# Kernel tuning notes

Hardware: AMD Instinct MI355X
Metric: run time of the kernel (lower is better)

The kernel has to match this reference:

```python
import jax, jax.numpy as jnp
import numpy as np
from jax.scipy.special import logsumexp

F = 200000   # numFactors
V = 100000   # numVars
S = 5        # state_dimensions (binary vars -> factor tables are (2,)*S)
E = 1000000  # number of factor-to-variable edges


def setup_inputs() -> dict:
    key = jax.random.key(0)
    ks = jax.random.split(key, 8)
    shape_f = (F,) + (2,) * S
    return {
        "factor_beliefs": jax.random.normal(ks[0], shape_f, jnp.float32),
        "var_beliefs": jax.random.normal(ks[1], (V, 2), jnp.float32),
        "factor_potentials": jax.random.normal(ks[2], shape_f, jnp.float32),
        "prv_varToFactor_messages": jax.random.normal(ks[3], (E, 2), jnp.float32),
        "prv_factorToVar_messages": jax.random.normal(ks[4], (E, 2), jnp.float32),
        "f2v_factor_idx": jax.random.randint(ks[5], (E,), 0, F),
        "f2v_var_idx": jax.random.randint(ks[6], (E,), 0, V),
        "edge_var_idx": jax.random.randint(ks[7], (E,), 0, S),
    }


def _bp_iteration(factor_beliefs, var_beliefs, factor_potentials,
                  prv_v2f, prv_f2v, f_idx, v_idx, ev_idx):
    nF = factor_beliefs.shape[0]
    nV = var_beliefs.shape[0]
    nS = factor_beliefs.ndim - 1  # state_dimensions

    # ---- message_factorToVar ----
    mapped_f = factor_beliefs[f_idx]  # [E, 2,...,2] gather along edges
    # logsumexp over all factor axes except each candidate axis d -> [E, S, 2]
    lse_per_axis = jnp.stack(
        [logsumexp(mapped_f, axis=tuple(a for a in range(1, nS + 1) if a != d + 1))
         for d in range(nS)], axis=1)
    # pick per-edge the axis this edge's variable occupies -> [E, 2]
    marg = jnp.take_along_axis(lse_per_axis, ev_idx[:, None, None], axis=1)[:, 0, :]
    f2v_msgs = marg - jnp.where(jnp.isneginf(prv_v2f), 0.0, prv_v2f)

    # ---- var beliefs: scatter-add over edges, then per-var normalization ----
    var_b = jax.ops.segment_sum(f2v_msgs, v_idx, num_segments=nV)
    var_b = var_b - logsumexp(var_b, axis=1, keepdims=True)

    # ---- message_varToFactor ----
    mapped_v = var_b[v_idx]  # [E, 2]
    v2f_msgs = mapped_v - jnp.where(jnp.isneginf(prv_f2v), 0.0, prv_f2v)

    # ---- expand each [2] message along its per-edge factor axis -> [E, 2^S] ----
    # expanded[e, i0..i_{S-1}] = msg[e, i_{ev_idx[e]}]
    idx_grid = jnp.indices((2,) * nS).reshape(nS, -1)  # [S, 2^S] coord along each axis
    sel = idx_grid[ev_idx]                              # [E, 2^S]
    expanded = jnp.take_along_axis(v2f_msgs, sel, axis=1)  # [E, 2^S]

    # ---- factor beliefs: scatter-add, add potentials, normalize per factor ----
    fb = jax.ops.segment_sum(expanded, f_idx, num_segments=nF)
    fb = fb.reshape((nF,) + (2,) * nS) + factor_potentials
    fb_flat = fb.reshape(nF, -1)
    fb = (fb_flat - logsumexp(fb_flat, axis=1, keepdims=True)).reshape(fb.shape)

    return var_b, fb, f2v_msgs, v2f_msgs


def reference(factor_beliefs, var_beliefs, factor_potentials,
              prv_varToFactor_messages, prv_factorToVar_messages,
              f2v_factor_idx, f2v_var_idx, edge_var_idx):
    # Returns (new var_beliefs, new factor_beliefs,
    #          prv_factorToVar_messages', prv_varToFactor_messages')
    return _bp_iteration(factor_beliefs, var_beliefs, factor_potentials,
                         prv_varToFactor_messages, prv_factorToVar_messages,
                         f2v_factor_idx, f2v_var_idx, edge_var_idx)
```

## Files before the change

kernel.cpp:

```cpp
#include <hip/hip_runtime.h>
#include <math.h>

__global__ void __launch_bounds__(256) k0_flse(
    const float* __restrict__ fbel,
    float* __restrict__ flse,
    int F)
{
    int f = blockIdx.x * 256 + threadIdx.x;
    if (f >= F) return;

    const float4* tab = reinterpret_cast<const float4*>(fbel + (size_t)f * 32);
    float v[32];
#pragma unroll
    for (int q = 0; q < 8; ++q) {
        float4 t = tab[q];
        v[q*4+0] = t.x; v[q*4+1] = t.y; v[q*4+2] = t.z; v[q*4+3] = t.w;
    }

    float m = v[0];
#pragma unroll
    for (int j = 1; j < 32; ++j) m = fmaxf(m, v[j]);

    float s[10];
#pragma unroll
    for (int i = 0; i < 10; ++i) s[i] = 0.f;
#pragma unroll
    for (int j = 0; j < 32; ++j) {
        float ex = __expf(v[j] - m);
#pragma unroll
        for (int d = 0; d < 5; ++d) s[d*2 + ((j >> (4 - d)) & 1)] += ex;
    }

    float* o = flse + (size_t)f * 10;
#pragma unroll
    for (int i = 0; i < 10; ++i) o[i] = m + __logf(s[i]);
}

__global__ void __launch_bounds__(256) k1_f2v(
    const float* __restrict__ flse,
    const float* __restrict__ pv2f,
    const int*   __restrict__ fidx,
    const int*   __restrict__ vidx,
    const int*   __restrict__ evidx,
    float* __restrict__ f2v_out,
    float* __restrict__ vacc,
    int E)
{
    int e = blockIdx.x * 256 + threadIdx.x;
    if (e >= E) return;
    int f = fidx[e], d = evidx[e];

    float2 lse = *reinterpret_cast<const float2*>(flse + (size_t)f * 10 + d * 2);
    float2 p   = *reinterpret_cast<const float2*>(pv2f + 2 * (size_t)e);
    float p0 = (p.x == -INFINITY) ? 0.f : p.x;
    float p1 = (p.y == -INFINITY) ? 0.f : p.y;
    float r0 = lse.x - p0, r1 = lse.y - p1;

    *reinterpret_cast<float2*>(f2v_out + 2 * (size_t)e) = make_float2(r0, r1);

    int vi = vidx[e];
    atomicAdd(&vacc[2*vi],   r0);
    atomicAdd(&vacc[2*vi+1], r1);
}

__global__ void __launch_bounds__(256) k2_varnorm(float* __restrict__ vb, int V)
{
    int v = blockIdx.x * 256 + threadIdx.x;
    if (v >= V) return;
    float a0 = vb[2*v], a1 = vb[2*v+1];
    float m = fmaxf(a0, a1);
    float l = m + __logf(__expf(a0 - m) + __expf(a1 - m));
    vb[2*v]   = a0 - l;
    vb[2*v+1] = a1 - l;
}

__global__ void __launch_bounds__(256) k3_v2f(
    const float* __restrict__ vb,
    const float* __restrict__ pf2v,
    const int*   __restrict__ fidx,
    const int*   __restrict__ vidx,
    const int*   __restrict__ evidx,
    float* __restrict__ v2f_out,
    float* __restrict__ facc,
    int E)
{
    int e = blockIdx.x * 256 + threadIdx.x;
    if (e >= E) return;
    int vi = vidx[e];
    float2 b = *reinterpret_cast<const float2*>(vb + 2 * (size_t)vi);
    float2 p = *reinterpret_cast<const float2*>(pf2v + 2 * (size_t)e);
    float p0 = (p.x == -INFINITY) ? 0.f : p.x;
    float p1 = (p.y == -INFINITY) ? 0.f : p.y;
    float r0 = b.x - p0, r1 = b.y - p1;

    *reinterpret_cast<float2*>(v2f_out + 2 * (size_t)e) = make_float2(r0, r1);

    int f = fidx[e], d = evidx[e];
    atomicAdd(&facc[(size_t)f*10 + d*2    ], r0);
    atomicAdd(&facc[(size_t)f*10 + d*2 + 1], r1);
}

__global__ void __launch_bounds__(256) k4_fb(
    const float* __restrict__ facc,
    const float* __restrict__ pot,
    float* __restrict__ fb_out,
    int F)
{
    int f = blockIdx.x * 256 + threadIdx.x;
    if (f >= F) return;

    float a[10];
#pragma unroll
    for (int i = 0; i < 10; ++i) a[i] = facc[(size_t)f*10 + i];

    float t[32];
    const float4* pp = reinterpret_cast<const float4*>(pot + (size_t)f * 32);
#pragma unroll
    for (int q = 0; q < 8; ++q) {
        float4 x = pp[q];
        t[q*4+0] = x.x; t[q*4+1] = x.y; t[q*4+2] = x.z; t[q*4+3] = x.w;
    }

    float m = -INFINITY;
#pragma unroll
    for (int j = 0; j < 32; ++j) {
        float s = t[j];
#pragma unroll
        for (int d = 0; d < 5; ++d) s += a[d*2 + ((j >> (4 - d)) & 1)];
        t[j] = s;
        m = fmaxf(m, s);
    }
    float sum = 0.f;
#pragma unroll
    for (int j = 0; j < 32; ++j) sum += __expf(t[j] - m);
    float l = m + __logf(sum);

    float4* out = reinterpret_cast<float4*>(fb_out + (size_t)f * 32);
#pragma unroll
    for (int q = 0; q < 8; ++q) {
        float4 x;
        x.x = t[q*4+0] - l; x.y = t[q*4+1] - l;
        x.z = t[q*4+2] - l; x.w = t[q*4+3] - l;
        out[q] = x;
    }
}

extern "C" void kernel_launch(void* const* d_in, const int* in_sizes, int n_in,
                              void* d_out, int out_size, void* d_ws, size_t ws_size,
                              hipStream_t stream)
{
    const float* fbel  = (const float*)d_in[0];
    const float* pot   = (const float*)d_in[2];
    const float* pv2f  = (const float*)d_in[3];
    const float* pf2v  = (const float*)d_in[4];
    const int*   fidx  = (const int*)d_in[5];
    const int*   vidx  = (const int*)d_in[6];
    const int*   evidx = (const int*)d_in[7];

    const int E  = in_sizes[5];
    const int F_ = in_sizes[0] / 32;
    const int V_ = in_sizes[1] / 2;

    float* out     = (float*)d_out;
    float* var_out = out;
    float* fb_out  = out + (size_t)V_ * 2;
    float* f2v_out = fb_out + (size_t)F_ * 32;
    float* v2f_out = f2v_out + (size_t)E * 2;

    float* flse = v2f_out;
    float* facc = (float*)d_ws;

    hipMemsetAsync(var_out, 0, (size_t)V_ * 2 * sizeof(float), stream);
    hipMemsetAsync(facc,    0, (size_t)F_ * 10 * sizeof(float), stream);

    k0_flse   <<<dim3((F_ + 255) / 256), dim3(256), 0, stream>>>(fbel, flse, F_);
    k1_f2v    <<<dim3((E  + 255) / 256), dim3(256), 0, stream>>>(
        flse, pv2f, fidx, vidx, evidx, f2v_out, var_out, E);
    k2_varnorm<<<dim3((V_ + 255) / 256), dim3(256), 0, stream>>>(var_out, V_);
    k3_v2f    <<<dim3((E  + 255) / 256), dim3(256), 0, stream>>>(
        var_out, pf2v, fidx, vidx, evidx, v2f_out, facc, E);
    k4_fb     <<<dim3((F_ + 255) / 256), dim3(256), 0, stream>>>(
        facc, pot, fb_out, F_);
}
```

Measured before the change: 347.8 us.

## Replicate scatter accumulators per XCC and use workgroup-scope atomics

Gives each XCC (read from the hardware register) its own copy of the variable and factor accumulators. The scatter atomics then run at workgroup scope, so they can resolve in the XCC-local L2 instead of being made coherent across the whole device. The normalization kernels sum the 8 replicas before normalizing. In exchange the zero-fill of the workspace grows eightfold and the reduce kernels read eight times more data. Correctness depends on workgroup-scope global atomics from different workgroups on the same XCC staying coherent in L2. The new path is taken only when the workspace is large enough.

```diff
diff --git a/kernel.cpp b/kernel.cpp
--- a/kernel.cpp
+++ b/kernel.cpp
@@ -1,5 +1,18 @@
 #include <hip/hip_runtime.h>
 #include <math.h>
+
+__device__ __forceinline__ int xcc_id() {
+    int x;
+    asm volatile("s_getreg_b32 %0, hwreg(HW_REG_XCC_ID)" : "=s"(x));
+    return x & 7;
+}
+
+__device__ __forceinline__ void atom_add(float* p, float v, int use_local) {
+    if (use_local)
+        __hip_atomic_fetch_add(p, v, __ATOMIC_RELAXED, __HIP_MEMORY_SCOPE_WORKGROUP);
+    else
+        __hip_atomic_fetch_add(p, v, __ATOMIC_RELAXED, __HIP_MEMORY_SCOPE_AGENT);
+}
 
 __global__ void __launch_bounds__(256) k0_flse(
     const float* __restrict__ fbel,
@@ -43,13 +56,16 @@
     const int*   __restrict__ vidx,
     const int*   __restrict__ evidx,
     float* __restrict__ f2v_out,
-    float* __restrict__ vacc,
+    float* __restrict__ vacc_rep,
+    long  vstride,
+    int   use_local,
     int E)
 {
     int e = blockIdx.x * 256 + threadIdx.x;
     if (e >= E) return;
+    float* vacc = vacc_rep + (use_local ? (size_t)xcc_id() * vstride : 0);
+
     int f = fidx[e], d = evidx[e];
-
     float2 lse = *reinterpret_cast<const float2*>(flse + (size_t)f * 10 + d * 2);
     float2 p   = *reinterpret_cast<const float2*>(pv2f + 2 * (size_t)e);
     float p0 = (p.x == -INFINITY) ? 0.f : p.x;
@@ -59,19 +75,26 @@
     *reinterpret_cast<float2*>(f2v_out + 2 * (size_t)e) = make_float2(r0, r1);
 
     int vi = vidx[e];
-    atomicAdd(&vacc[2*vi],   r0);
-    atomicAdd(&vacc[2*vi+1], r1);
-}
-
-__global__ void __launch_bounds__(256) k2_varnorm(float* __restrict__ vb, int V)
+    atom_add(&vacc[2 * (size_t)vi],     r0, use_local);
+    atom_add(&vacc[2 * (size_t)vi + 1], r1, use_local);
+}
+
+__global__ void __launch_bounds__(256) k2_varnorm(
+    const float* __restrict__ vacc_rep,
+    float* __restrict__ var_out,
+    int V, int R, long vstride)
 {
     int v = blockIdx.x * 256 + threadIdx.x;
     if (v >= V) return;
-    float a0 = vb[2*v], a1 = vb[2*v+1];
+    float a0 = 0.f, a1 = 0.f;
+    for (int r = 0; r < R; ++r) {
+        float2 t = *reinterpret_cast<const float2*>(vacc_rep + (size_t)r * vstride + 2 * (size_t)v);
+        a0 += t.x; a1 += t.y;
+    }
     float m = fmaxf(a0, a1);
     float l = m + __logf(__expf(a0 - m) + __expf(a1 - m));
-    vb[2*v]   = a0 - l;
-    vb[2*v+1] = a1 - l;
+    var_out[2*v]   = a0 - l;
+    var_out[2*v+1] = a1 - l;
 }
 
 __global__ void __launch_bounds__(256) k3_v2f(
@@ -81,11 +104,15 @@
     const int*   __restrict__ vidx,
     const int*   __restrict__ evidx,
     float* __restrict__ v2f_out,
-    float* __restrict__ facc,
+    float* __restrict__ facc_rep,
+    long  fstride,
+    int   use_local,
     int E)
 {
     int e = blockIdx.x * 256 + threadIdx.x;
     if (e >= E) return;
+    float* facc = facc_rep + (use_local ? (size_t)xcc_id() * fstride : 0);
+
     int vi = vidx[e];
     float2 b = *reinterpret_cast<const float2*>(vb + 2 * (size_t)vi);
     float2 p = *reinterpret_cast<const float2*>(pf2v + 2 * (size_t)e);
@@ -96,22 +123,27 @@
     *reinterpret_cast<float2*>(v2f_out + 2 * (size_t)e) = make_float2(r0, r1);
 
     int f = fidx[e], d = evidx[e];
-    atomicAdd(&facc[(size_t)f*10 + d*2    ], r0);
-    atomicAdd(&facc[(size_t)f*10 + d*2 + 1], r1);
+    atom_add(&facc[(size_t)f * 10 + d * 2],     r0, use_local);
+    atom_add(&facc[(size_t)f * 10 + d * 2 + 1], r1, use_local);
 }
 
 __global__ void __launch_bounds__(256) k4_fb(
-    const float* __restrict__ facc,
+    const float* __restrict__ facc_rep,
     const float* __restrict__ pot,
     float* __restrict__ fb_out,
-    int F)
+    int F, int R, long fstride)
 {
     int f = blockIdx.x * 256 + threadIdx.x;
     if (f >= F) return;
 
     float a[10];
 #pragma unroll
-    for (int i = 0; i < 10; ++i) a[i] = facc[(size_t)f*10 + i];
+    for (int i = 0; i < 10; ++i) a[i] = 0.f;
+    for (int r = 0; r < R; ++r) {
+        const float* src = facc_rep + (size_t)r * fstride + (size_t)f * 10;
+#pragma unroll
+        for (int i = 0; i < 10; ++i) a[i] += src[i];
+    }
 
     float t[32];
     const float4* pp = reinterpret_cast<const float4*>(pot + (size_t)f * 32);
@@ -168,17 +200,25 @@
     float* v2f_out = f2v_out + (size_t)E * 2;
 
     float* flse = v2f_out;
-    float* facc = (float*)d_ws;
-
-    hipMemsetAsync(var_out, 0, (size_t)V_ * 2 * sizeof(float), stream);
-    hipMemsetAsync(facc,    0, (size_t)F_ * 10 * sizeof(float), stream);
+
+    const long V2  = (long)V_ * 2;
+    const long F10 = (long)F_ * 10;
+
+    int R = (ws_size >= (size_t)8 * (size_t)(V2 + F10) * sizeof(float)) ? 8 : 1;
+    int use_local = (R == 8) ? 1 : 0;
+    float* vacc_rep = (float*)d_ws;
+    float* facc_rep = vacc_rep + (size_t)R * V2;
+
+    (void)hipMemsetAsync(d_ws, 0, (size_t)R * (size_t)(V2 + F10) * sizeof(float),
+                         stream);
 
     k0_flse   <<<dim3((F_ + 255) / 256), dim3(256), 0, stream>>>(fbel, flse, F_);
     k1_f2v    <<<dim3((E  + 255) / 256), dim3(256), 0, stream>>>(
-        flse, pv2f, fidx, vidx, evidx, f2v_out, var_out, E);
-    k2_varnorm<<<dim3((V_ + 255) / 256), dim3(256), 0, stream>>>(var_out, V_);
+        flse, pv2f, fidx, vidx, evidx, f2v_out, vacc_rep, V2, use_local, E);
+    k2_varnorm<<<dim3((V_ + 255) / 256), dim3(256), 0, stream>>>(
+        vacc_rep, var_out, V_, R, V2);
     k3_v2f    <<<dim3((E  + 255) / 256), dim3(256), 0, stream>>>(
-        var_out, pf2v, fidx, vidx, evidx, v2f_out, facc, E);
+        var_out, pf2v, fidx, vidx, evidx, v2f_out, facc_rep, F10, use_local, E);
     k4_fb     <<<dim3((F_ + 255) / 256), dim3(256), 0, stream>>>(
-        facc, pot, fb_out, F_);
-}
+        facc_rep, pot, fb_out, F_, R, F10);
+}
```

Measured after the change: 366.5 us. +5.4%, slower.

## Replicate var accumulators per XCC with narrow-scope atomics; coarsen v2f kernel

Applied to the files above, without the earlier changes.

The variable-belief scatter-add now goes into eight per-XCC replicas of the accumulator, stored in the not-yet-written factor-belief output buffer. Each replica is updated with relaxed wavefront-scope atomics, and the variable-normalization kernel sums the eight replicas. The goal is to keep atomics inside each XCC's own L2 and avoid cross-die coherence traffic. The v2f kernel also processes four edges per thread and uses explicit agent-scope relaxed atomics. The cost is an 8x larger memset plus extra reads in the reduction, and correctness relies on wavefront-scope atomics still being resolved at the shared L2.

```diff
diff --git a/kernel.cpp b/kernel.cpp
--- a/kernel.cpp
+++ b/kernel.cpp
@@ -1,5 +1,19 @@
 #include <hip/hip_runtime.h>
 #include <math.h>
+
+__device__ __forceinline__ int xcc_id() {
+    int x;
+    asm volatile("s_getreg_b32 %0, hwreg(HW_REG_XCC_ID)" : "=s"(x));
+    return x & 7;
+}
+
+__device__ __forceinline__ void atom_add_l2(float* p, float v) {
+    __hip_atomic_fetch_add(p, v, __ATOMIC_RELAXED, __HIP_MEMORY_SCOPE_WAVEFRONT);
+}
+
+__device__ __forceinline__ void atom_add_dev(float* p, float v) {
+    __hip_atomic_fetch_add(p, v, __ATOMIC_RELAXED, __HIP_MEMORY_SCOPE_AGENT);
+}
 
 __global__ void __launch_bounds__(256) k0_flse(
     const float* __restrict__ fbel,
@@ -43,13 +57,15 @@
     const int*   __restrict__ vidx,
     const int*   __restrict__ evidx,
     float* __restrict__ f2v_out,
-    float* __restrict__ vacc,
+    float* __restrict__ vacc_rep,
+    long  vstride,
     int E)
 {
     int e = blockIdx.x * 256 + threadIdx.x;
     if (e >= E) return;
+    float* vacc = vacc_rep + (size_t)xcc_id() * vstride;
+
     int f = fidx[e], d = evidx[e];
-
     float2 lse = *reinterpret_cast<const float2*>(flse + (size_t)f * 10 + d * 2);
     float2 p   = *reinterpret_cast<const float2*>(pv2f + 2 * (size_t)e);
     float p0 = (p.x == -INFINITY) ? 0.f : p.x;
@@ -59,19 +75,28 @@
     *reinterpret_cast<float2*>(f2v_out + 2 * (size_t)e) = make_float2(r0, r1);
 
     int vi = vidx[e];
-    atomicAdd(&vacc[2*vi],   r0);
-    atomicAdd(&vacc[2*vi+1], r1);
-}
-
-__global__ void __launch_bounds__(256) k2_varnorm(float* __restrict__ vb, int V)
+    atom_add_l2(&vacc[2 * (size_t)vi],     r0);
+    atom_add_l2(&vacc[2 * (size_t)vi + 1], r1);
+}
+
+__global__ void __launch_bounds__(256) k2_varnorm(
+    const float* __restrict__ vacc_rep,
+    float* __restrict__ var_out,
+    int V, long vstride)
 {
     int v = blockIdx.x * 256 + threadIdx.x;
     if (v >= V) return;
-    float a0 = vb[2*v], a1 = vb[2*v+1];
+    float a0 = 0.f, a1 = 0.f;
+#pragma unroll
+    for (int r = 0; r < 8; ++r) {
+        float2 t = *reinterpret_cast<const float2*>(
+            vacc_rep + (size_t)r * vstride + 2 * (size_t)v);
+        a0 += t.x; a1 += t.y;
+    }
     float m = fmaxf(a0, a1);
     float l = m + __logf(__expf(a0 - m) + __expf(a1 - m));
-    vb[2*v]   = a0 - l;
-    vb[2*v+1] = a1 - l;
+    var_out[2*v]   = a0 - l;
+    var_out[2*v+1] = a1 - l;
 }
 
 __global__ void __launch_bounds__(256) k3_v2f(
@@ -84,20 +109,25 @@
     float* __restrict__ facc,
     int E)
 {
-    int e = blockIdx.x * 256 + threadIdx.x;
-    if (e >= E) return;
-    int vi = vidx[e];
-    float2 b = *reinterpret_cast<const float2*>(vb + 2 * (size_t)vi);
-    float2 p = *reinterpret_cast<const float2*>(pf2v + 2 * (size_t)e);
-    float p0 = (p.x == -INFINITY) ? 0.f : p.x;
-    float p1 = (p.y == -INFINITY) ? 0.f : p.y;
-    float r0 = b.x - p0, r1 = b.y - p1;
-
-    *reinterpret_cast<float2*>(v2f_out + 2 * (size_t)e) = make_float2(r0, r1);
-
-    int f = fidx[e], d = evidx[e];
-    atomicAdd(&facc[(size_t)f*10 + d*2    ], r0);
-    atomicAdd(&facc[(size_t)f*10 + d*2 + 1], r1);
+    int base = blockIdx.x * 1024 + threadIdx.x;
+#pragma unroll
+    for (int i = 0; i < 4; ++i) {
+        int e = base + i * 256;
+        if (e >= E) continue;
+
+        int vi = vidx[e];
+        float2 b = *reinterpret_cast<const float2*>(vb + 2 * (size_t)vi);
+        float2 p = *reinterpret_cast<const float2*>(pf2v + 2 * (size_t)e);
+        float p0 = (p.x == -INFINITY) ? 0.f : p.x;
+        float p1 = (p.y == -INFINITY) ? 0.f : p.y;
+        float r0 = b.x - p0, r1 = b.y - p1;
+
+        *reinterpret_cast<float2*>(v2f_out + 2 * (size_t)e) = make_float2(r0, r1);
+
+        int f = fidx[e], d = evidx[e];
+        atom_add_dev(&facc[(size_t)f * 10 + d * 2],     r0);
+        atom_add_dev(&facc[(size_t)f * 10 + d * 2 + 1], r1);
+    }
 }
 
 __global__ void __launch_bounds__(256) k4_fb(
@@ -111,7 +141,7 @@
 
     float a[10];
 #pragma unroll
-    for (int i = 0; i < 10; ++i) a[i] = facc[(size_t)f*10 + i];
+    for (int i = 0; i < 10; ++i) a[i] = facc[(size_t)f * 10 + i];
 
     float t[32];
     const float4* pp = reinterpret_cast<const float4*>(pot + (size_t)f * 32);
@@ -168,16 +198,22 @@
     float* v2f_out = f2v_out + (size_t)E * 2;
 
     float* flse = v2f_out;
-    float* facc = (float*)d_ws;
-
-    hipMemsetAsync(var_out, 0, (size_t)V_ * 2 * sizeof(float), stream);
-    hipMemsetAsync(facc,    0, (size_t)F_ * 10 * sizeof(float), stream);
+
+    const long V2  = (long)V_ * 2;
+    const long F10 = (long)F_ * 10;
+
+    float* vacc_rep = fb_out;
+    float* facc     = (float*)d_ws;
+
+    (void)hipMemsetAsync(vacc_rep, 0, (size_t)8 * V2 * sizeof(float), stream);
+    (void)hipMemsetAsync(facc,     0, (size_t)F10 * sizeof(float), stream);
 
     k0_flse   <<<dim3((F_ + 255) / 256), dim3(256), 0, stream>>>(fbel, flse, F_);
     k1_f2v    <<<dim3((E  + 255) / 256), dim3(256), 0, stream>>>(
-        flse, pv2f, fidx, vidx, evidx, f2v_out, var_out, E);
-    k2_varnorm<<<dim3((V_ + 255) / 256), dim3(256), 0, stream>>>(var_out, V_);
-    k3_v2f    <<<dim3((E  + 255) / 256), dim3(256), 0, stream>>>(
+        flse, pv2f, fidx, vidx, evidx, f2v_out, vacc_rep, V2, E);
+    k2_varnorm<<<dim3((V_ + 255) / 256), dim3(256), 0, stream>>>(
+        vacc_rep, var_out, V_, V2);
+    k3_v2f    <<<dim3((E  + 1023) / 1024), dim3(256), 0, stream>>>(
         var_out, pf2v, fidx, vidx, evidx, v2f_out, facc, E);
     k4_fb     <<<dim3((F_ + 255) / 256), dim3(256), 0, stream>>>(
         facc, pot, fb_out, F_);
```

Result: no change. 348.3 us (+0.1%).
